# Kernel optimization log

Measured on AMD Instinct MI355X. Metric: run time of the kernel, lower is better.

The kernel has to match this reference:

```python
import jax, jax.numpy as jnp
import numpy as np

N_NODES = 50000
N_EDGES = 800000
IN_CH = 128
HIDDEN = 32
HEADS = 4
OUT_CH = 128


def _lin_params(key, fan_in, fan_out):
    kw, kb = jax.random.split(key)
    scale = 1.0 / np.sqrt(fan_in)
    W = jax.random.uniform(kw, (fan_in, fan_out), minval=-scale, maxval=scale, dtype=jnp.float32)
    b = jax.random.uniform(kb, (fan_out,), minval=-scale, maxval=scale, dtype=jnp.float32)
    return W, b


def setup_inputs() -> dict:
    key = jax.random.key(0)
    ks = jax.random.split(key, 10)
    x = jax.random.normal(ks[0], (N_NODES, IN_CH), dtype=jnp.float32)
    edge_index = jax.random.randint(ks[1], (2, N_EDGES), 0, N_NODES, dtype=jnp.int64)
    d1 = HIDDEN * HEADS  # 128
    Wq1, bq1 = _lin_params(ks[2], IN_CH, d1)
    Wk1, bk1 = _lin_params(ks[3], IN_CH, d1)
    Wv1, bv1 = _lin_params(ks[4], IN_CH, d1)
    Ws1, bs1 = _lin_params(ks[5], IN_CH, d1)
    Wq2, bq2 = _lin_params(ks[6], d1, OUT_CH)
    Wk2, bk2 = _lin_params(ks[7], d1, OUT_CH)
    Wv2, bv2 = _lin_params(ks[8], d1, OUT_CH)
    Ws2, bs2 = _lin_params(ks[9], d1, OUT_CH)
    return dict(x=x, edge_index=edge_index,
                Wq1=Wq1, bq1=bq1, Wk1=Wk1, bk1=bk1, Wv1=Wv1, bv1=bv1, Ws1=Ws1, bs1=bs1,
                Wq2=Wq2, bq2=bq2, Wk2=Wk2, bk2=bk2, Wv2=Wv2, bv2=bv2, Ws2=Ws2, bs2=bs2)


def transformer_conv(x, src, dst, Wq, bq, Wk, bk, Wv, bv, Ws, bs, heads, n_nodes):
    """PyG TransformerConv (concat=True, beta=False, root_weight=True, dropout=0)."""
    H = heads
    d = Wq.shape[1] // H
    q = (x @ Wq + bq).reshape(n_nodes, H, d)  # [N,H,d]
    k = (x @ Wk + bk).reshape(n_nodes, H, d)
    v = (x @ Wv + bv).reshape(n_nodes, H, d)
    q_e = q[dst]          # [E,H,d] gather by destination (x_i)
    k_e = k[src]          # [E,H,d] gather by source (x_j)
    alpha = jnp.einsum('ehd,ehd->eh', q_e, k_e) / jnp.sqrt(jnp.float32(d))  # [E,H]
    # segment softmax over incoming edges of each destination node
    m = jax.ops.segment_max(alpha, dst, num_segments=n_nodes)  # [N,H]
    m = jnp.where(jnp.isfinite(m), m, 0.0)
    e = jnp.exp(alpha - m[dst])
    denom = jax.ops.segment_sum(e, dst, num_segments=n_nodes)  # [N,H]
    attn = e / (denom[dst] + 1e-16)                            # [E,H]
    msg = v[src] * attn[:, :, None]                            # [E,H,d]
    out = jax.ops.segment_sum(msg, dst, num_segments=n_nodes)  # [N,H,d]
    out = out.reshape(n_nodes, H * d)
    return out + (x @ Ws + bs)  # root/skip connection


def reference(x, edge_index, Wq1, bq1, Wk1, bk1, Wv1, bv1, Ws1, bs1,
              Wq2, bq2, Wk2, bk2, Wv2, bv2, Ws2, bs2):
    src = edge_index[0]
    dst = edge_index[1]
    n = x.shape[0]
    h = transformer_conv(x, src, dst, Wq1, bq1, Wk1, bk1, Wv1, bv1, Ws1, bs1, HEADS, n)
    h = jax.nn.relu(h)
    out = transformer_conv(h, src, dst, Wq2, bq2, Wk2, bk2, Wv2, bv2, Ws2, bs2, 1, n)
    return out
```

## Files before the change

kernel.cpp:

```cpp
#include <hip/hip_runtime.h>

#define N_NODES 50000
#define N_EDGES 800000

typedef __attribute__((ext_vector_type(8))) short bf16x8;
typedef __attribute__((ext_vector_type(4))) float f32x4;

__device__ inline unsigned short f2bf(float f) {
  unsigned int u = __float_as_uint(f);
  unsigned int r = u + 0x7FFFu + ((u >> 16) & 1u);
  return (unsigned short)(r >> 16);
}

__global__ void detect_i64(const int* __restrict__ ei, int* __restrict__ flag) {
  int t = threadIdx.x;
  int v = ei[2 * t + 1];
  unsigned long long b = __ballot(v == 0);
  if (t == 0) *flag = (b == 0xFFFFFFFFFFFFFFFFull) ? 1 : 0;
}

__global__ void edges_prep(const int* __restrict__ ei, const int* __restrict__ flag,
                           int* __restrict__ src, int* __restrict__ dst,
                           int* __restrict__ cnt) {
  int e = blockIdx.x * 256 + threadIdx.x;
  if (e >= N_EDGES) return;
  int s, d;
  if (*flag) { s = ei[2 * e]; d = ei[2 * (N_EDGES + e)]; }
  else       { s = ei[e];     d = ei[N_EDGES + e]; }
  src[e] = s; dst[e] = d;
  atomicAdd(&cnt[d], 1);
}

__device__ inline int block_excl_scan_256(int v, int& total) {
  __shared__ int lds[8];
  int lane = threadIdx.x & 63, wid = threadIdx.x >> 6;
  int orig = v;
#pragma unroll
  for (int off = 1; off < 64; off <<= 1) {
    int t = __shfl_up(v, off);
    if (lane >= off) v += t;
  }
  if (lane == 63) lds[wid] = v;
  __syncthreads();
  if (threadIdx.x == 0) {
    int s = 0;
    for (int w = 0; w < 4; ++w) { int t = lds[w]; lds[w] = s; s += t; }
    lds[4] = s;
  }
  __syncthreads();
  total = lds[4];
  return v + lds[wid] - orig;
}

__global__ __launch_bounds__(256) void scan1(const int* __restrict__ cnt,
                                             int* __restrict__ excl,
                                             int* __restrict__ partials) {
  int i = blockIdx.x * 256 + threadIdx.x;
  int v = (i < N_NODES) ? cnt[i] : 0;
  int total;
  int e = block_excl_scan_256(v, total);
  if (i < N_NODES) excl[i] = e;
  if (threadIdx.x == 0) partials[blockIdx.x] = total;
}

__global__ __launch_bounds__(256) void scan2(int* __restrict__ partials, int nb) {
  int i = threadIdx.x;
  int v = (i < nb) ? partials[i] : 0;
  int total;
  int e = block_excl_scan_256(v, total);
  if (i < nb) partials[i] = e;
}

__global__ __launch_bounds__(256) void scan3(int* __restrict__ row_ptr,
                                             const int* __restrict__ partials,
                                             int* __restrict__ cursor) {
  int i = blockIdx.x * 256 + threadIdx.x;
  if (i < N_NODES) {
    int v = row_ptr[i] + partials[blockIdx.x];
    row_ptr[i] = v;
    cursor[i] = v;
  }
  if (i == 0) row_ptr[N_NODES] = N_EDGES;
}

__global__ void scatter_k(const int* __restrict__ src, const int* __restrict__ dst,
                          int* __restrict__ cursor, int* __restrict__ ssrc) {
  int e = blockIdx.x * 256 + threadIdx.x;
  if (e < N_EDGES) {
    int p = atomicAdd(&cursor[dst[e]], 1);
    ssrc[p] = src[e];
  }
}

__global__ void f32_to_bf16_vec(const float* __restrict__ in, unsigned short* __restrict__ out) {
  int i = blockIdx.x * 256 + threadIdx.x;
  float4 v = ((const float4*)in)[i];
  ushort4 o;
  o.x = f2bf(v.x); o.y = f2bf(v.y); o.z = f2bf(v.z); o.w = f2bf(v.w);
  ((ushort4*)out)[i] = o;
}

__global__ void prep_w(const float* __restrict__ Wq, const float* __restrict__ bq,
                       const float* __restrict__ Wk, const float* __restrict__ bk,
                       const float* __restrict__ Wv, const float* __restrict__ bv,
                       const float* __restrict__ Ws, const float* __restrict__ bs,
                       unsigned short* __restrict__ bt, float* __restrict__ bcat) {
  int t = blockIdx.x * 256 + threadIdx.x;
  int col = t >> 7, kk = t & 127;
  int sel = col >> 7, c = col & 127;
  const float* W = (sel == 0) ? Wq : (sel == 1) ? Wk : (sel == 2) ? Wv : Ws;
  bt[col * 128 + kk] = f2bf(W[kk * 128 + c]);
  if (kk == 0) {
    const float* B = (sel == 0) ? bq : (sel == 1) ? bk : (sel == 2) ? bv : bs;
    bcat[col] = B[c];
  }
}

__global__ __launch_bounds__(256) void gemm_qkvs(const unsigned short* __restrict__ xb,
                                                 const unsigned short* __restrict__ bt,
                                                 const float* __restrict__ bias,
                                                 float* __restrict__ Oq,
                                                 unsigned short* __restrict__ Okv,
                                                 float* __restrict__ Os) {
  const int wid = threadIdx.x >> 6;
  const int lane = threadIdx.x & 63;
  const int gw = blockIdx.x * 4 + wid;
  const int colGroup = gw & 7;
  const int rowGroup = gw >> 3;
  const int col0 = colGroup * 64;
  const int r = lane & 15;
  const int half = lane >> 4;

  bf16x8 bfrag[4][4];
#pragma unroll
  for (int ct = 0; ct < 4; ++ct) {
    int col = col0 + ct * 16 + r;
    const unsigned short* bp = bt + col * 128 + half * 8;
#pragma unroll
    for (int kc = 0; kc < 4; ++kc)
      bfrag[ct][kc] = *(const bf16x8*)(bp + kc * 32);
  }

#pragma unroll 1
  for (int rt = 0; rt < 5; ++rt) {
    int m0 = (rowGroup * 5 + rt) * 16;
    const unsigned short* ap = xb + (size_t)(m0 + r) * 128 + half * 8;
    bf16x8 afrag[4];
#pragma unroll
    for (int kc = 0; kc < 4; ++kc) afrag[kc] = *(const bf16x8*)(ap + kc * 32);
    f32x4 acc[4] = {{0.f,0.f,0.f,0.f},{0.f,0.f,0.f,0.f},{0.f,0.f,0.f,0.f},{0.f,0.f,0.f,0.f}};
#pragma unroll
    for (int ct = 0; ct < 4; ++ct)
#pragma unroll
      for (int kc = 0; kc < 4; ++kc)
        acc[ct] = __builtin_amdgcn_mfma_f32_16x16x32_bf16(afrag[kc], bfrag[ct][kc], acc[ct], 0, 0, 0);

    int orow = m0 + half * 4;
    if (colGroup < 2) {
#pragma unroll
      for (int ct = 0; ct < 4; ++ct) {
        int col = col0 + ct * 16 + r;
        float bv = bias[col];
#pragma unroll
        for (int j = 0; j < 4; ++j)
          Oq[(size_t)(orow + j) * 128 + col] = acc[ct][j] + bv;
      }
    } else if (colGroup >= 6) {
#pragma unroll
      for (int ct = 0; ct < 4; ++ct) {
        int col = col0 + ct * 16 + r;
        float bv = bias[col];
        int c = col - 384;
#pragma unroll
        for (int j = 0; j < 4; ++j)
          Os[(size_t)(orow + j) * 128 + c] = acc[ct][j] + bv;
      }
    } else {
      const int voff  = (colGroup >= 4) ? 2 : 0;
      const int cbase = (colGroup >= 4) ? 256 : 128;
#pragma unroll
      for (int ct = 0; ct < 4; ++ct) {
        int col = col0 + ct * 16 + r;
        float bv = bias[col];
        int c = col - cbase;
        int pos = ((c >> 1) << 2) + voff + (c & 1);
#pragma unroll
        for (int j = 0; j < 4; ++j)
          Okv[(size_t)(orow + j) * 256 + pos] = f2bf(acc[ct][j] + bv);
      }
    }
  }
}

template <int H, bool OUTBF>
__global__ __launch_bounds__(256) void edge_attn(const float* __restrict__ Oq,
                                                 const unsigned short* __restrict__ Okv,
                                                 const float* __restrict__ Os,
                                                 const int* __restrict__ row_ptr,
                                                 const int* __restrict__ ssrc,
                                                 void* __restrict__ outp,
                                                 float scale) {
  int wid = threadIdx.x >> 6, lane = threadIdx.x & 63;
  int n = blockIdx.x * 4 + wid;
  if (n >= N_NODES) return;
  const float2 q2 = *(const float2*)(Oq + (size_t)n * 128 + 2 * lane);
  float qx = q2.x * scale, qy = q2.y * scale;
  int start = row_ptr[n], end = row_ptr[n + 1];
  int len = end - start;
  const int* sp = ssrc + start;
  const uint2* kvb = (const uint2*)Okv;
  float acc0 = 0.f, acc1 = 0.f, den = 0.f;

  auto proc = [&](uint2 kv) {
    float k0 = __uint_as_float(kv.x << 16);
    float k1 = __uint_as_float(kv.x & 0xffff0000u);
    float p = qx * k0 + qy * k1;
#pragma unroll
    for (int off = 1; off < 64 / H; off <<= 1) p += __shfl_xor(p, off);
    float e = __expf(p);
    float v0 = __uint_as_float(kv.y << 16);
    float v1 = __uint_as_float(kv.y & 0xffff0000u);
    den += e; acc0 += e * v0; acc1 += e * v1;
  };

  if (len >= 2) {
    int sA = sp[0], sB = sp[1];
    uint2 kvA = kvb[(size_t)sA * 64 + lane];
    uint2 kvB = kvb[(size_t)sB * 64 + lane];
    for (int i = 2; i < len; ++i) {
      int sN = sp[i];
      uint2 kvN = kvb[(size_t)sN * 64 + lane];
      proc(kvA);
      kvA = kvB; kvB = kvN;
    }
    proc(kvA); proc(kvB);
  } else if (len == 1) {
    proc(kvb[(size_t)sp[0] * 64 + lane]);
  }

  float inv = 1.0f / (den + 1e-16f);
  float2 sk = *(const float2*)(Os + (size_t)n * 128 + 2 * lane);
  float r0 = acc0 * inv + sk.x;
  float r1 = acc1 * inv + sk.y;
  if (OUTBF) {
    r0 = fmaxf(r0, 0.f); r1 = fmaxf(r1, 0.f);
    unsigned int pk = (unsigned int)f2bf(r0) | ((unsigned int)f2bf(r1) << 16);
    ((unsigned int*)outp)[(size_t)n * 64 + lane] = pk;
  } else {
    ((float2*)outp)[(size_t)n * 64 + lane] = make_float2(r0, r1);
  }
}

extern "C" void kernel_launch(void* const* d_in, const int* in_sizes, int n_in,
                              void* d_out, int out_size, void* d_ws, size_t ws_size,
                              hipStream_t stream) {
  (void)in_sizes; (void)n_in; (void)out_size; (void)ws_size;
  const float* x  = (const float*)d_in[0];
  const int*   ei = (const int*)d_in[1];
  const float *Wq1 = (const float*)d_in[2],  *bq1 = (const float*)d_in[3];
  const float *Wk1 = (const float*)d_in[4],  *bk1 = (const float*)d_in[5];
  const float *Wv1 = (const float*)d_in[6],  *bv1 = (const float*)d_in[7];
  const float *Ws1 = (const float*)d_in[8],  *bs1 = (const float*)d_in[9];
  const float *Wq2 = (const float*)d_in[10], *bq2 = (const float*)d_in[11];
  const float *Wk2 = (const float*)d_in[12], *bk2 = (const float*)d_in[13];
  const float *Wv2 = (const float*)d_in[14], *bv2 = (const float*)d_in[15];
  const float *Ws2 = (const float*)d_in[16], *bs2 = (const float*)d_in[17];
  float* out = (float*)d_out;

  char* w = (char*)d_ws;
  size_t off = 0;
  auto alloc = [&](size_t b) { void* p = w + off; off += (b + 255) & ~(size_t)255; return p; };
  int* flag   = (int*)alloc(4);
  int* src    = (int*)alloc((size_t)N_EDGES * 4);
  int* dstA   = (int*)alloc((size_t)N_EDGES * 4);
  int* ssrc   = (int*)alloc((size_t)N_EDGES * 4);
  int* rowp   = (int*)alloc((size_t)(N_NODES + 1) * 4);
  int* cursor = (int*)alloc((size_t)N_NODES * 4);
  int* cnt    = (int*)alloc((size_t)N_NODES * 4);
  int* part   = (int*)alloc(256 * 4);
  unsigned short* xb = (unsigned short*)alloc((size_t)N_NODES * 128 * 2);
  unsigned short* bt = (unsigned short*)alloc((size_t)512 * 128 * 2);
  float* bcat = (float*)alloc(512 * 4);
  float* Oq   = (float*)alloc((size_t)N_NODES * 128 * 4);
  unsigned short* Okv = (unsigned short*)alloc((size_t)N_NODES * 256 * 2);
  float* Os   = (float*)alloc((size_t)N_NODES * 128 * 4);

  hipMemsetAsync(cnt, 0, (size_t)N_NODES * 4, stream);
  detect_i64<<<1, 64, 0, stream>>>(ei, flag);
  edges_prep<<<3125, 256, 0, stream>>>(ei, flag, src, dstA, cnt);
  scan1<<<196, 256, 0, stream>>>(cnt, rowp, part);
  scan2<<<1, 256, 0, stream>>>(part, 196);
  scan3<<<196, 256, 0, stream>>>(rowp, part, cursor);
  scatter_k<<<3125, 256, 0, stream>>>(src, dstA, cursor, ssrc);

  f32_to_bf16_vec<<<6250, 256, 0, stream>>>(x, xb);
  prep_w<<<256, 256, 0, stream>>>(Wq1, bq1, Wk1, bk1, Wv1, bv1, Ws1, bs1, bt, bcat);
  gemm_qkvs<<<1250, 256, 0, stream>>>(xb, bt, bcat, Oq, Okv, Os);
  edge_attn<4, true><<<12500, 256, 0, stream>>>(Oq, Okv, Os, rowp, ssrc, xb, 0.17677669529663689f);

  prep_w<<<256, 256, 0, stream>>>(Wq2, bq2, Wk2, bk2, Wv2, bv2, Ws2, bs2, bt, bcat);
  gemm_qkvs<<<1250, 256, 0, stream>>>(xb, bt, bcat, Oq, Okv, Os);
  edge_attn<1, false><<<12500, 256, 0, stream>>>(Oq, Okv, Os, rowp, ssrc, out, 0.08838834764831845f);
}
```

Before: 436.2 us.

## Fuse input conversion and scans, store Q/skip as bf16, deepen edge prefetch

Fuses the f32-to-bf16 conversion of x into the first GEMM's A-fragment load, folds int64 detection into edges_prep, and replaces the three-kernel scan with a single 1024-thread block scan. Q and skip outputs are now stored as interleaved bf16 instead of fp32, which halves their write and read traffic. The edge-attention loop now prefetches four neighbours at a time instead of two. This removes several launches and a full pass over x, at the cost of lower Q/skip precision and a serial single-block scan.

```diff
diff --git a/kernel.cpp b/kernel.cpp
--- a/kernel.cpp
+++ b/kernel.cpp
@@ -11,76 +11,54 @@
   unsigned int r = u + 0x7FFFu + ((u >> 16) & 1u);
   return (unsigned short)(r >> 16);
 }
-
-__global__ void detect_i64(const int* __restrict__ ei, int* __restrict__ flag) {
-  int t = threadIdx.x;
-  int v = ei[2 * t + 1];
-  unsigned long long b = __ballot(v == 0);
-  if (t == 0) *flag = (b == 0xFFFFFFFFFFFFFFFFull) ? 1 : 0;
-}
-
-__global__ void edges_prep(const int* __restrict__ ei, const int* __restrict__ flag,
+__device__ inline float bf_lo(unsigned int u) { return __uint_as_float(u << 16); }
+__device__ inline float bf_hi(unsigned int u) { return __uint_as_float(u & 0xffff0000u); }
+
+__global__ void edges_prep(const int* __restrict__ ei,
                            int* __restrict__ src, int* __restrict__ dst,
                            int* __restrict__ cnt) {
   int e = blockIdx.x * 256 + threadIdx.x;
-  if (e >= N_EDGES) return;
+  int hi = ei[2 * e + 1];
+  unsigned long long b = __ballot(hi == 0);
+  bool is64 = (b == 0xFFFFFFFFFFFFFFFFull);
   int s, d;
-  if (*flag) { s = ei[2 * e]; d = ei[2 * (N_EDGES + e)]; }
-  else       { s = ei[e];     d = ei[N_EDGES + e]; }
+  if (is64) { s = ei[2 * e]; d = ei[2 * (N_EDGES + e)]; }
+  else      { s = ei[e];     d = ei[N_EDGES + e]; }
   src[e] = s; dst[e] = d;
   atomicAdd(&cnt[d], 1);
 }
 
-__device__ inline int block_excl_scan_256(int v, int& total) {
-  __shared__ int lds[8];
-  int lane = threadIdx.x & 63, wid = threadIdx.x >> 6;
-  int orig = v;
+__global__ __launch_bounds__(1024) void scan_all(const int* __restrict__ cnt,
+                                                 int* __restrict__ rowp,
+                                                 int* __restrict__ cursor) {
+  __shared__ int wpre[16];
+  const int PER = 49;
+  int t = threadIdx.x;
+  int lane = t & 63, wid = t >> 6;
+  int base = t * PER;
+  int lim = base + PER; if (lim > N_NODES) lim = N_NODES;
+  int s = 0;
+  for (int i = base; i < lim; ++i) s += cnt[i];
+  int v = s;
 #pragma unroll
   for (int off = 1; off < 64; off <<= 1) {
-    int t = __shfl_up(v, off);
-    if (lane >= off) v += t;
-  }
-  if (lane == 63) lds[wid] = v;
+    int u = __shfl_up(v, off);
+    if (lane >= off) v += u;
+  }
+  if (lane == 63) wpre[wid] = v;
   __syncthreads();
-  if (threadIdx.x == 0) {
-    int s = 0;
-    for (int w = 0; w < 4; ++w) { int t = lds[w]; lds[w] = s; s += t; }
-    lds[4] = s;
+  if (t == 0) {
+    int acc = 0;
+    for (int w = 0; w < 16; ++w) { int u = wpre[w]; wpre[w] = acc; acc += u; }
   }
   __syncthreads();
-  total = lds[4];
-  return v + lds[wid] - orig;
-}
-
-__global__ __launch_bounds__(256) void scan1(const int* __restrict__ cnt,
-                                             int* __restrict__ excl,
-                                             int* __restrict__ partials) {
-  int i = blockIdx.x * 256 + threadIdx.x;
-  int v = (i < N_NODES) ? cnt[i] : 0;
-  int total;
-  int e = block_excl_scan_256(v, total);
-  if (i < N_NODES) excl[i] = e;
-  if (threadIdx.x == 0) partials[blockIdx.x] = total;
-}
-
-__global__ __launch_bounds__(256) void scan2(int* __restrict__ partials, int nb) {
-  int i = threadIdx.x;
-  int v = (i < nb) ? partials[i] : 0;
-  int total;
-  int e = block_excl_scan_256(v, total);
-  if (i < nb) partials[i] = e;
-}
-
-__global__ __launch_bounds__(256) void scan3(int* __restrict__ row_ptr,
-                                             const int* __restrict__ partials,
-                                             int* __restrict__ cursor) {
-  int i = blockIdx.x * 256 + threadIdx.x;
-  if (i < N_NODES) {
-    int v = row_ptr[i] + partials[blockIdx.x];
-    row_ptr[i] = v;
-    cursor[i] = v;
-  }
-  if (i == 0) row_ptr[N_NODES] = N_EDGES;
+  int run = v - s + wpre[wid];
+  for (int i = base; i < lim; ++i) {
+    int c = cnt[i];
+    rowp[i] = run; cursor[i] = run;
+    run += c;
+  }
+  if (t == 0) rowp[N_NODES] = N_EDGES;
 }
 
 __global__ void scatter_k(const int* __restrict__ src, const int* __restrict__ dst,
@@ -90,14 +68,6 @@
     int p = atomicAdd(&cursor[dst[e]], 1);
     ssrc[p] = src[e];
   }
-}
-
-__global__ void f32_to_bf16_vec(const float* __restrict__ in, unsigned short* __restrict__ out) {
-  int i = blockIdx.x * 256 + threadIdx.x;
-  float4 v = ((const float4*)in)[i];
-  ushort4 o;
-  o.x = f2bf(v.x); o.y = f2bf(v.y); o.z = f2bf(v.z); o.w = f2bf(v.w);
-  ((ushort4*)out)[i] = o;
 }
 
 __global__ void prep_w(const float* __restrict__ Wq, const float* __restrict__ bq,
@@ -116,12 +86,12 @@
   }
 }
 
-__global__ __launch_bounds__(256) void gemm_qkvs(const unsigned short* __restrict__ xb,
+template <bool AF32>
+__global__ __launch_bounds__(256) void gemm_qkvs(const void* __restrict__ xa,
                                                  const unsigned short* __restrict__ bt,
                                                  const float* __restrict__ bias,
-                                                 float* __restrict__ Oq,
-                                                 unsigned short* __restrict__ Okv,
-                                                 float* __restrict__ Os) {
+                                                 unsigned short* __restrict__ Oqs,
+                                                 unsigned short* __restrict__ Okv) {
   const int wid = threadIdx.x >> 6;
   const int lane = threadIdx.x & 63;
   const int gw = blockIdx.x * 4 + wid;
@@ -144,10 +114,26 @@
 #pragma unroll 1
   for (int rt = 0; rt < 5; ++rt) {
     int m0 = (rowGroup * 5 + rt) * 16;
-    const unsigned short* ap = xb + (size_t)(m0 + r) * 128 + half * 8;
     bf16x8 afrag[4];
-#pragma unroll
-    for (int kc = 0; kc < 4; ++kc) afrag[kc] = *(const bf16x8*)(ap + kc * 32);
+    if constexpr (AF32) {
+      const float* ap = (const float*)xa + (size_t)(m0 + r) * 128 + half * 8;
+#pragma unroll
+      for (int kc = 0; kc < 4; ++kc) {
+        float4 f0 = *(const float4*)(ap + kc * 32);
+        float4 f1 = *(const float4*)(ap + kc * 32 + 4);
+        bf16x8 fr;
+        fr[0] = (short)f2bf(f0.x); fr[1] = (short)f2bf(f0.y);
+        fr[2] = (short)f2bf(f0.z); fr[3] = (short)f2bf(f0.w);
+        fr[4] = (short)f2bf(f1.x); fr[5] = (short)f2bf(f1.y);
+        fr[6] = (short)f2bf(f1.z); fr[7] = (short)f2bf(f1.w);
+        afrag[kc] = fr;
+      }
+    } else {
+      const unsigned short* ap = (const unsigned short*)xa + (size_t)(m0 + r) * 128 + half * 8;
+#pragma unroll
+      for (int kc = 0; kc < 4; ++kc) afrag[kc] = *(const bf16x8*)(ap + kc * 32);
+    }
+
     f32x4 acc[4] = {{0.f,0.f,0.f,0.f},{0.f,0.f,0.f,0.f},{0.f,0.f,0.f,0.f},{0.f,0.f,0.f,0.f}};
 #pragma unroll
     for (int ct = 0; ct < 4; ++ct)
@@ -163,7 +149,7 @@
         float bv = bias[col];
 #pragma unroll
         for (int j = 0; j < 4; ++j)
-          Oq[(size_t)(orow + j) * 128 + col] = acc[ct][j] + bv;
+          Oqs[(size_t)(orow + j) * 256 + col] = f2bf(acc[ct][j] + bv);
       }
     } else if (colGroup >= 6) {
 #pragma unroll
@@ -173,7 +159,7 @@
         int c = col - 384;
 #pragma unroll
         for (int j = 0; j < 4; ++j)
-          Os[(size_t)(orow + j) * 128 + c] = acc[ct][j] + bv;
+          Oqs[(size_t)(orow + j) * 256 + 128 + c] = f2bf(acc[ct][j] + bv);
       }
     } else {
       const int voff  = (colGroup >= 4) ? 2 : 0;
@@ -193,9 +179,8 @@
 }
 
 template <int H, bool OUTBF>
-__global__ __launch_bounds__(256) void edge_attn(const float* __restrict__ Oq,
+__global__ __launch_bounds__(256) void edge_attn(const unsigned short* __restrict__ Oqs,
                                                  const unsigned short* __restrict__ Okv,
-                                                 const float* __restrict__ Os,
                                                  const int* __restrict__ row_ptr,
                                                  const int* __restrict__ ssrc,
                                                  void* __restrict__ outp,
@@ -203,8 +188,9 @@
   int wid = threadIdx.x >> 6, lane = threadIdx.x & 63;
   int n = blockIdx.x * 4 + wid;
   if (n >= N_NODES) return;
-  const float2 q2 = *(const float2*)(Oq + (size_t)n * 128 + 2 * lane);
-  float qx = q2.x * scale, qy = q2.y * scale;
+  const unsigned int* qsw = (const unsigned int*)Oqs;
+  unsigned int qw = qsw[(size_t)n * 128 + lane];
+  float qx = bf_lo(qw) * scale, qy = bf_hi(qw) * scale;
   int start = row_ptr[n], end = row_ptr[n + 1];
   int len = end - start;
   const int* sp = ssrc + start;
@@ -212,36 +198,35 @@
   float acc0 = 0.f, acc1 = 0.f, den = 0.f;
 
   auto proc = [&](uint2 kv) {
-    float k0 = __uint_as_float(kv.x << 16);
-    float k1 = __uint_as_float(kv.x & 0xffff0000u);
-    float p = qx * k0 + qy * k1;
+    float p = qx * bf_lo(kv.x) + qy * bf_hi(kv.x);
 #pragma unroll
     for (int off = 1; off < 64 / H; off <<= 1) p += __shfl_xor(p, off);
     float e = __expf(p);
-    float v0 = __uint_as_float(kv.y << 16);
-    float v1 = __uint_as_float(kv.y & 0xffff0000u);
-    den += e; acc0 += e * v0; acc1 += e * v1;
+    den += e; acc0 += e * bf_lo(kv.y); acc1 += e * bf_hi(kv.y);
   };
 
-  if (len >= 2) {
-    int sA = sp[0], sB = sp[1];
-    uint2 kvA = kvb[(size_t)sA * 64 + lane];
-    uint2 kvB = kvb[(size_t)sB * 64 + lane];
-    for (int i = 2; i < len; ++i) {
-      int sN = sp[i];
-      uint2 kvN = kvb[(size_t)sN * 64 + lane];
-      proc(kvA);
-      kvA = kvB; kvB = kvN;
+  int i = 0;
+  if (len >= 4) {
+    uint2 a = kvb[(size_t)sp[0] * 64 + lane];
+    uint2 b = kvb[(size_t)sp[1] * 64 + lane];
+    uint2 c = kvb[(size_t)sp[2] * 64 + lane];
+    uint2 d = kvb[(size_t)sp[3] * 64 + lane];
+    for (i = 4; i + 3 < len; i += 4) {
+      uint2 na = kvb[(size_t)sp[i]     * 64 + lane];
+      uint2 nb = kvb[(size_t)sp[i + 1] * 64 + lane];
+      uint2 nc = kvb[(size_t)sp[i + 2] * 64 + lane];
+      uint2 nd = kvb[(size_t)sp[i + 3] * 64 + lane];
+      proc(a); proc(b); proc(c); proc(d);
+      a = na; b = nb; c = nc; d = nd;
     }
-    proc(kvA); proc(kvB);
-  } else if (len == 1) {
-    proc(kvb[(size_t)sp[0] * 64 + lane]);
-  }
+    proc(a); proc(b); proc(c); proc(d);
+  }
+  for (; i < len; ++i) proc(kvb[(size_t)sp[i] * 64 + lane]);
 
   float inv = 1.0f / (den + 1e-16f);
-  float2 sk = *(const float2*)(Os + (size_t)n * 128 + 2 * lane);
-  float r0 = acc0 * inv + sk.x;
-  float r1 = acc1 * inv + sk.y;
+  unsigned int sw = qsw[(size_t)n * 128 + 64 + lane];
+  float r0 = acc0 * inv + bf_lo(sw);
+  float r1 = acc1 * inv + bf_hi(sw);
   if (OUTBF) {
     r0 = fmaxf(r0, 0.f); r1 = fmaxf(r1, 0.f);
     unsigned int pk = (unsigned int)f2bf(r0) | ((unsigned int)f2bf(r1) << 16);
@@ -270,35 +255,28 @@
   char* w = (char*)d_ws;
   size_t off = 0;
   auto alloc = [&](size_t b) { void* p = w + off; off += (b + 255) & ~(size_t)255; return p; };
-  int* flag   = (int*)alloc(4);
   int* src    = (int*)alloc((size_t)N_EDGES * 4);
   int* dstA   = (int*)alloc((size_t)N_EDGES * 4);
   int* ssrc   = (int*)alloc((size_t)N_EDGES * 4);
   int* rowp   = (int*)alloc((size_t)(N_NODES + 1) * 4);
   int* cursor = (int*)alloc((size_t)N_NODES * 4);
   int* cnt    = (int*)alloc((size_t)N_NODES * 4);
-  int* part   = (int*)alloc(256 * 4);
-  unsigned short* xb = (unsigned short*)alloc((size_t)N_NODES * 128 * 2);
-  unsigned short* bt = (unsigned short*)alloc((size_t)512 * 128 * 2);
+  unsigned short* xb  = (unsigned short*)alloc((size_t)N_NODES * 128 * 2);
+  unsigned short* bt  = (unsigned short*)alloc((size_t)512 * 128 * 2);
   float* bcat = (float*)alloc(512 * 4);
-  float* Oq   = (float*)alloc((size_t)N_NODES * 128 * 4);
+  unsigned short* Oqs = (unsigned short*)alloc((size_t)N_NODES * 256 * 2);
   unsigned short* Okv = (unsigned short*)alloc((size_t)N_NODES * 256 * 2);
-  float* Os   = (float*)alloc((size_t)N_NODES * 128 * 4);
 
   hipMemsetAsync(cnt, 0, (size_t)N_NODES * 4, stream);
-  detect_i64<<<1, 64, 0, stream>>>(ei, flag);
-  edges_prep<<<3125, 256, 0, stream>>>(ei, flag, src, dstA, cnt);
-  scan1<<<196, 256, 0, stream>>>(cnt, rowp, part);
-  scan2<<<1, 256, 0, stream>>>(part, 196);
-  scan3<<<196, 256, 0, stream>>>(rowp, part, cursor);
+  edges_prep<<<3125, 256, 0, stream>>>(ei, src, dstA, cnt);
+  scan_all<<<1, 1024, 0, stream>>>(cnt, rowp, cursor);
   scatter_k<<<3125, 256, 0, stream>>>(src, dstA, cursor, ssrc);
 
-  f32_to_bf16_vec<<<6250, 256, 0, stream>>>(x, xb);
   prep_w<<<256, 256, 0, stream>>>(Wq1, bq1, Wk1, bk1, Wv1, bv1, Ws1, bs1, bt, bcat);
-  gemm_qkvs<<<1250, 256, 0, stream>>>(xb, bt, bcat, Oq, Okv, Os);
-  edge_attn<4, true><<<12500, 256, 0, stream>>>(Oq, Okv, Os, rowp, ssrc, xb, 0.17677669529663689f);
+  gemm_qkvs<true><<<1250, 256, 0, stream>>>(x, bt, bcat, Oqs, Okv);
+  edge_attn<4, true><<<12500, 256, 0, stream>>>(Oqs, Okv, rowp, ssrc, xb, 0.17677669529663689f);
 
   prep_w<<<256, 256, 0, stream>>>(Wq2, bq2, Wk2, bk2, Wv2, bv2, Ws2, bs2, bt, bcat);
-  gemm_qkvs<<<1250, 256, 0, stream>>>(xb, bt, bcat, Oq, Okv, Os);
-  edge_attn<1, false><<<12500, 256, 0, stream>>>(Oq, Okv, Os, rowp, ssrc, out, 0.08838834764831845f);
-}
+  gemm_qkvs<false><<<1250, 256, 0, stream>>>(xb, bt, bcat, Oqs, Okv);
+  edge_attn<1, false><<<12500, 256, 0, stream>>>(Oqs, Okv, rowp, ssrc, out, 0.08838834764831845f);
+}
```

Result: slower. 510.7 us (+17.1%).
